# Kernel optimization log

Measured on AMD Instinct MI355X. Metric: run time of the kernel, lower is better.

## Reference

```python
import jax, jax.numpy as jnp
import numpy as np

B, S, H, W = 64, 32, 40, 64
SENS, UNITS, MOTOR, NA = 1283, 48, 4, 2
UNFOLDS = 6  # ncps LTC default ode_unfolds
EPS = 1e-8


def setup_inputs() -> dict:
    key = jax.random.key(0)
    ks = iter(jax.random.split(key, 40))
    u = lambda sh, lo, hi: jax.random.uniform(next(ks), sh, jnp.float32, lo, hi)
    inp = {}
    inp["depth_image"] = jax.random.uniform(next(ks), (B, S, H, W), jnp.float32)
    inp["relative_position"] = jax.random.normal(next(ks), (B, S, 3), jnp.float32)
    # CNN params (conv k3 s2 p1 + ReLU) x3: 1->32->64->32
    def cw(o, i):
        return jax.random.normal(next(ks), (o, i, 3, 3), jnp.float32) / np.sqrt(i * 9.0)
    inp["w1"], inp["b1"] = cw(32, 1), jnp.zeros((32,), jnp.float32)
    inp["w2"], inp["b2"] = cw(64, 32), jnp.zeros((64,), jnp.float32)
    inp["w3"], inp["b3"] = cw(32, 64), jnp.zeros((32,), jnp.float32)
    # LTC cell params (ncps init ranges)
    inp["input_w"] = jnp.ones((SENS,), jnp.float32)
    inp["input_b"] = jnp.zeros((SENS,), jnp.float32)
    inp["sens_w"] = u((SENS, UNITS), 0.001, 1.0)
    inp["sens_mu"] = u((SENS, UNITS), 0.3, 0.8)
    inp["sens_sigma"] = u((SENS, UNITS), 3.0, 8.0)
    inp["sens_erev"] = jnp.sign(jax.random.normal(next(ks), (SENS, UNITS)))
    inp["rec_w"] = u((UNITS, UNITS), 0.001, 1.0)
    inp["rec_mu"] = u((UNITS, UNITS), 0.3, 0.8)
    inp["rec_sigma"] = u((UNITS, UNITS), 3.0, 8.0)
    inp["rec_erev"] = jnp.sign(jax.random.normal(next(ks), (UNITS, UNITS)))
    inp["gleak"] = u((UNITS,), 0.001, 1.0)
    inp["vleak"] = u((UNITS,), -0.2, 0.2)
    inp["cm"] = u((UNITS,), 0.4, 0.6)
    inp["out_w"] = jnp.ones((MOTOR,), jnp.float32)
    inp["out_b"] = jnp.zeros((MOTOR,), jnp.float32)
    inp["head_w"] = jax.random.normal(next(ks), (MOTOR, NA), jnp.float32) * 0.5
    inp["head_b"] = jnp.zeros((NA,), jnp.float32)
    inp["sens_mask"] = (jax.random.uniform(next(ks), (SENS, UNITS)) < 0.3).astype(jnp.int32)
    inp["rec_mask"] = (jax.random.uniform(next(ks), (UNITS, UNITS)) < 0.3).astype(jnp.int32)
    return inp


def _conv(x, w, b):
    y = jax.lax.conv_general_dilated(x, w, (2, 2), [(1, 1), (1, 1)],
                                     dimension_numbers=("NCHW", "OIHW", "NCHW"))
    return jax.nn.relu(y + b[None, :, None, None])


def reference(depth_image, relative_position, w1, b1, w2, b2, w3, b3,
              input_w, input_b, sens_w, sens_mu, sens_sigma, sens_erev,
              rec_w, rec_mu, rec_sigma, rec_erev, gleak, vleak, cm,
              out_w, out_b, head_w, head_b, sens_mask, rec_mask):
    b, s = depth_image.shape[:2]
    x = depth_image.reshape(b * s, 1, H, W)
    x = _conv(_conv(_conv(x, w1, b1), w2, b2), w3, b3)  # [b*s,32,5,8]
    feat = x.reshape(b, s, -1)  # [b,s,1280]
    seq = jnp.concatenate([feat, relative_position.reshape(b, s, -1)], axis=2)  # [b,s,1283]

    sp = jax.nn.softplus
    smask = sens_mask.astype(seq.dtype)
    rmask = rec_mask.astype(seq.dtype)
    cm_t = sp(cm) * UNFOLDS          # cm / (elapsed_time / ode_unfolds), dt=1
    gl = sp(gleak)
    sw_pos = sp(sens_w) * smask
    rw_pos = sp(rec_w) * rmask

    def step(v, xt):  # xt: [b, SENS]
        I = xt * input_w + input_b
        # sensory synapse activations: [b, SENS, UNITS]
        sa = sw_pos * jax.nn.sigmoid(sens_sigma * (I[:, :, None] - sens_mu))
        w_num_s = (sa * sens_erev).sum(1)  # [b, UNITS]
        w_den_s = sa.sum(1)
        def unfold(v, _):
            ra = rw_pos * jax.nn.sigmoid(rec_sigma * (v[:, :, None] - rec_mu))
            num = cm_t * v + gl * vleak + (ra * rec_erev).sum(1) + w_num_s
            den = cm_t + gl + ra.sum(1) + w_den_s
            return num / (den + EPS), None
        v, _ = jax.lax.scan(unfold, v, None, length=UNFOLDS)
        y = v[:, :MOTOR] * out_w + out_b  # motor neuron readout
        return v, y

    v0 = jnp.zeros((b, UNITS), seq.dtype)
    _, ys = jax.lax.scan(step, v0, jnp.swapaxes(seq, 0, 1))  # [s, b, MOTOR]
    pooled = ys.mean(0)  # mean over seq dim
    return jnp.tanh(pooled @ head_w + head_b)  # [b, NA] action mean
```

## Files before the change

### kernel.cpp

```cpp
#include <hip/hip_runtime.h>
#include <hip/hip_bf16.h>


typedef __attribute__((ext_vector_type(8))) short bshort8;
typedef __attribute__((ext_vector_type(4))) float f32x4;

constexpr long OFF_SEQ  = 0;
constexpr long OFF_SP4  = 2627584;
constexpr long OFF_RP4  = 2873920;
constexpr long OFF_CM   = 2886208;
constexpr long OFF_W2B  = 2886400;
constexpr long OFF_W3B  = 2898688;
constexpr long OFF_PART = 2907904;

__device__ __forceinline__ float sp_(float x) {
    return fmaxf(x, 0.f) + log1pf(expf(-fabsf(x)));
}

__global__ void prep_kernel(const float* __restrict__ sens_w, const float* __restrict__ sens_mu,
                            const float* __restrict__ sens_sigma, const float* __restrict__ sens_erev,
                            const int* __restrict__ sens_mask,
                            const float* __restrict__ rec_w, const float* __restrict__ rec_mu,
                            const float* __restrict__ rec_sigma, const float* __restrict__ rec_erev,
                            const int* __restrict__ rec_mask,
                            const float* __restrict__ gleak, const float* __restrict__ vleak,
                            const float* __restrict__ cm,
                            const float* __restrict__ w2, const float* __restrict__ w3,
                            float* __restrict__ ws) {
    const float L2E = 1.4426950408889634f;
    int i = blockIdx.x * 256 + threadIdx.x;
    if (i < 61584) {
        float m  = sens_mask[i] ? 1.f : 0.f;
        float sw = sp_(sens_w[i]) * m;
        float sg = sens_sigma[i], mu = sens_mu[i];
        ((float4*)(ws + OFF_SP4))[i] =
            make_float4(-sg * L2E, sg * mu * L2E, sw * sens_erev[i], sw);
    } else if (i < 64656) {
        int q = i - 61584;
        int j = q >> 6, u = q & 63;
        float4 v = make_float4(0.f, 0.f, 0.f, 0.f);
        if (u < 48) {
            int idx = j * 48 + u;
            float m  = rec_mask[idx] ? 1.f : 0.f;
            float sw = sp_(rec_w[idx]) * m;
            float sg = rec_sigma[idx], mu = rec_mu[idx];
            v = make_float4(-sg * L2E, sg * mu * L2E, sw * rec_erev[idx], sw);
        }
        ((float4*)(ws + OFF_RP4))[q] = v;
    } else if (i < 64704) {
        int u = i - 64656;
        float g = sp_(gleak[u]);
        ws[OFF_CM + u]       = sp_(cm[u]) * 6.f;
        ws[OFF_CM + 64 + u]  = g;
        ws[OFF_CM + 128 + u] = g * vleak[u];
    } else if (i < 89280) {
        int n = i - 64704;
        int j = n & 7, l = (n >> 3) & 63, t2 = n >> 9;
        int wv = t2 & 3;
        int r  = t2 >> 2;
        int xp = r & 1, hk = r >> 1;
        int ky = hk % 3, h = hk / 3;
        int oc = wv * 16 + (l & 15);
        int kgB = l >> 4;
        int icl = (kgB & 1) * 8 + j;
        int ic = h * 16 + icl;
        int kx = 2 * xp + (kgB >> 1);
        float val = (kx == 3) ? 0.f : w2[((oc * 32 + ic) * 3 + ky) * 3 + kx];
        ((__hip_bfloat16*)(ws + OFF_W2B))[n] = __float2bfloat16(val);
    } else if (i < 107712) {
        int n = i - 89280;
        int j = n & 7, l = (n >> 3) & 63, t3 = n >> 9;
        int h = t3 & 1, u2 = t3 >> 1;
        int nt = u2 / 9, p = u2 % 9;
        int ky = p / 3, kx = p % 3;
        int oc = nt * 16 + (l & 15);
        int ic = h * 32 + (l >> 4) * 8 + j;
        ((__hip_bfloat16*)(ws + OFF_W3B))[n] =
            __float2bfloat16(w3[((oc * 64 + ic) * 3 + ky) * 3 + kx]);
    }
}

#define IMGB 0
#define C1H  5424
#define A2E  0
#define A2O  12672
#define SMB  28272

__global__ __launch_bounds__(256, 4) void cnn_kernel(
    const float* __restrict__ depth, const float* __restrict__ relpos,
    const float* __restrict__ w1, const float* __restrict__ b1,
    const float* __restrict__ b2, const float* __restrict__ b3,
    const __hip_bfloat16* __restrict__ w2b, const __hip_bfloat16* __restrict__ w3b,
    float* __restrict__ seq) {
    __shared__ __align__(16) char smraw[SMB];
    const int t = threadIdx.x;
    const int img = blockIdx.x;
    const int l = t & 63;
    const int wvu = __builtin_amdgcn_readfirstlane(t >> 6);
    const int m = l & 15, kg = l >> 4;

    for (int i = t; i < 7068; i += 256) ((uint*)smraw)[i] = 0u;
    __syncthreads();
    for (int i = t; i < 1280; i += 256) {
        int pos = 2 * i;
        int h = pos >> 6, w = pos & 63;
        float2 d = *(const float2*)(depth + (long)img * 2560 + pos);
        __hip_bfloat162 pk = __float22bfloat162_rn(d);
        *(__hip_bfloat162*)(smraw + IMGB + ((h + 1) * 66 + (w + 2)) * 2) = pk;
    }
    __syncthreads();

    const __hip_bfloat16* imgp = (const __hip_bfloat16*)(smraw + IMGB);
    f32x4 acc[10];
    {
        float bias = b2[wvu * 16 + m];
#pragma unroll
        for (int mt = 0; mt < 10; ++mt) acc[mt] = (f32x4){bias, bias, bias, bias};
    }

#pragma unroll 1
    for (int h = 0; h < 2; ++h) {
        const int ocb = h * 16 + wvu * 4;
        float wv4[4][9], bv4[4];
#pragma unroll
        for (int j = 0; j < 4; ++j) {
            bv4[j] = b1[ocb + j];
#pragma unroll
            for (int k = 0; k < 9; ++k) wv4[j][k] = w1[(ocb + j) * 9 + k];
        }
#pragma unroll 1
        for (int i = 0; i < 10; ++i) {
            int p = l + (i << 6);
            int y1 = p >> 5, x1 = p & 31;
            float xin[9];
#pragma unroll
            for (int ky = 0; ky < 3; ++ky)
#pragma unroll
                for (int kx = 0; kx < 3; ++kx)
                    xin[ky * 3 + kx] = __bfloat162float(imgp[(2 * y1 + ky) * 66 + 2 * x1 + kx + 1]);
            float o[4];
#pragma unroll
            for (int j = 0; j < 4; ++j) {
                float a = bv4[j];
#pragma unroll
                for (int k = 0; k < 9; ++k) a = fmaf(wv4[j][k], xin[k], a);
                o[j] = fmaxf(a, 0.f);
            }
            char* cb = smraw + C1H + (((y1 + 1) * 34) + (x1 + 1)) * 32 + wvu * 8;
            *(__hip_bfloat162*)cb       = __float22bfloat162_rn(make_float2(o[0], o[1]));
            *(__hip_bfloat162*)(cb + 4) = __float22bfloat162_rn(make_float2(o[2], o[3]));
        }
        bshort8 Bh[6];
#pragma unroll
        for (int f = 0; f < 6; ++f)
            Bh[f] = *(const bshort8*)(w2b + (((h * 6 + f) * 4 + wvu) * 64 + l) * 8);
        __syncthreads();
#pragma unroll
        for (int ky = 0; ky < 3; ++ky) {
#pragma unroll
            for (int xp = 0; xp < 2; ++xp) {
                bshort8 Bp = Bh[ky * 2 + xp];
                const char* base = smraw + C1H + (ky * 34 + 2 * m + 2 * xp + (kg >> 1)) * 32 + (kg & 1) * 16;
#pragma unroll
                for (int mt = 0; mt < 10; ++mt) {
                    bshort8 A = *(const bshort8*)(base + mt * 2176);
                    acc[mt] = __builtin_amdgcn_mfma_f32_16x16x32_bf16(A, Bp, acc[mt], 0, 0, 0);
                }
            }
        }
        __syncthreads();
    }

    for (int i = t; i < 6336; i += 256) ((uint*)smraw)[i] = 0u;
    __syncthreads();
    {
        int oc = wvu * 16 + m;
        int q = oc >> 3, sub = oc & 7;
#pragma unroll
        for (int mt = 0; mt < 10; ++mt) {
            int row = mt + 1;
#pragma unroll
            for (int reg = 0; reg < 4; ++reg) {
                int x2 = kg * 4 + reg;
                int odd = x2 & 1;
                int xi = odd ? ((x2 + 1) >> 1) : (x2 >> 1);
                char* ab = smraw + (odd ? A2O : A2E);
                float v = fmaxf(acc[mt][reg], 0.f);
                *(__hip_bfloat16*)(ab + (((q * 11 + row) * 9 + xi) * 8 + sub) * 2) = __float2bfloat16(v);
            }
        }
    }
    __syncthreads();

    {
        const int nt = wvu & 1;
        const bool two = wvu < 2;
        f32x4 c3a = (f32x4){0.f, 0.f, 0.f, 0.f};
        f32x4 c3b = (f32x4){0.f, 0.f, 0.f, 0.f};
        const int xb = m & 7, yb = m >> 3;
#pragma unroll
        for (int p = 0; p < 9; ++p) {
            int ky = p / 3, kx = p % 3;
            const char* arr = smraw + ((kx == 1) ? A2E : A2O);
            int xi3 = xb + (kx == 2);
#pragma unroll
            for (int h = 0; h < 2; ++h) {
                bshort8 B = *(const bshort8*)(w3b + (((nt * 9 + p) * 2 + h) * 64 + l) * 8);
                int q = h * 4 + kg;
                const char* base = arr + ((q * 11 + 2 * yb + ky) * 9 + xi3) * 16;
                if (two) {
                    bshort8 A0 = *(const bshort8*)(base);
                    c3a = __builtin_amdgcn_mfma_f32_16x16x32_bf16(A0, B, c3a, 0, 0, 0);
                    bshort8 A2 = *(const bshort8*)(base + 1152);
                    c3b = __builtin_amdgcn_mfma_f32_16x16x32_bf16(A2, B, c3b, 0, 0, 0);
                } else {
                    bshort8 A1 = *(const bshort8*)(base + 576);
                    c3a = __builtin_amdgcn_mfma_f32_16x16x32_bf16(A1, B, c3a, 0, 0, 0);
                }
            }
        }
        __syncthreads();
        float* sb = (float*)smraw;
        int oc = nt * 16 + m;
        float bv = b3[oc];
        int ob40 = oc * 40;
        if (two) {
#pragma unroll
            for (int reg = 0; reg < 4; ++reg) {
                sb[ob40 + kg * 4 + reg] = fmaxf(c3a[reg] + bv, 0.f);
                int px2 = 32 + kg * 4 + reg;
                if (px2 < 40) sb[ob40 + px2] = fmaxf(c3b[reg] + bv, 0.f);
            }
        } else {
#pragma unroll
            for (int reg = 0; reg < 4; ++reg)
                sb[ob40 + 16 + kg * 4 + reg] = fmaxf(c3a[reg] + bv, 0.f);
        }
        __syncthreads();
        for (int i = t; i < 1283; i += 256)
            seq[(long)img * 1283 + i] = (i < 1280) ? sb[i] : relpos[img * 3 + (i - 1280)];
    }
}

__global__ __launch_bounds__(768) void sensory_kernel(
    const float* __restrict__ sp, const float* __restrict__ seq,
    const float* __restrict__ iw, const float* __restrict__ ibias,
    float2* __restrict__ part) {
    const float4* P4 = (const float4*)sp;
    __shared__ __align__(16) char sbuf[49152];
    float*  IT  = (float*)sbuf;
    float2* red = (float2*)sbuf;
    const int t = threadIdx.x;
    const int pb = blockIdx.x * 8;

    for (int p = 0; p < 8; ++p)
        for (int k = t; k < 1283; k += 768)
            IT[k * 8 + p] = fmaf(seq[(long)(pb + p) * 1283 + k], iw[k], ibias[k]);
    __syncthreads();

    const int u = t % 48, kg = t / 48;
    float2 acc[8];
#pragma unroll
    for (int p = 0; p < 8; ++p) acc[p] = make_float2(0.f, 0.f);

#pragma unroll 2
    for (int i = 0; i < 81; ++i) {
        int k = kg + 16 * i;
        if (k < 1283) {
            float4 pv = P4[k * 48 + u];
            float4 Ia = *(const float4*)&IT[k * 8];
            float4 Ib = *(const float4*)&IT[k * 8 + 4];
            float r0 = __builtin_amdgcn_rcpf(1.f + __builtin_amdgcn_exp2f(fmaf(pv.x, Ia.x, pv.y)));
            float r1 = __builtin_amdgcn_rcpf(1.f + __builtin_amdgcn_exp2f(fmaf(pv.x, Ia.y, pv.y)));
            float r2 = __builtin_amdgcn_rcpf(1.f + __builtin_amdgcn_exp2f(fmaf(pv.x, Ia.z, pv.y)));
            float r3 = __builtin_amdgcn_rcpf(1.f + __builtin_amdgcn_exp2f(fmaf(pv.x, Ia.w, pv.y)));
            float r4 = __builtin_amdgcn_rcpf(1.f + __builtin_amdgcn_exp2f(fmaf(pv.x, Ib.x, pv.y)));
            float r5 = __builtin_amdgcn_rcpf(1.f + __builtin_amdgcn_exp2f(fmaf(pv.x, Ib.y, pv.y)));
            float r6 = __builtin_amdgcn_rcpf(1.f + __builtin_amdgcn_exp2f(fmaf(pv.x, Ib.z, pv.y)));
            float r7 = __builtin_amdgcn_rcpf(1.f + __builtin_amdgcn_exp2f(fmaf(pv.x, Ib.w, pv.y)));
            acc[0].x = fmaf(pv.z, r0, acc[0].x); acc[0].y = fmaf(pv.w, r0, acc[0].y);
            acc[1].x = fmaf(pv.z, r1, acc[1].x); acc[1].y = fmaf(pv.w, r1, acc[1].y);
            acc[2].x = fmaf(pv.z, r2, acc[2].x); acc[2].y = fmaf(pv.w, r2, acc[2].y);
            acc[3].x = fmaf(pv.z, r3, acc[3].x); acc[3].y = fmaf(pv.w, r3, acc[3].y);
            acc[4].x = fmaf(pv.z, r4, acc[4].x); acc[4].y = fmaf(pv.w, r4, acc[4].y);
            acc[5].x = fmaf(pv.z, r5, acc[5].x); acc[5].y = fmaf(pv.w, r5, acc[5].y);
            acc[6].x = fmaf(pv.z, r6, acc[6].x); acc[6].y = fmaf(pv.w, r6, acc[6].y);
            acc[7].x = fmaf(pv.z, r7, acc[7].x); acc[7].y = fmaf(pv.w, r7, acc[7].y);
        }
    }
    __syncthreads();
#pragma unroll
    for (int p = 0; p < 8; ++p) red[(kg * 8 + p) * 48 + u] = acc[p];
    __syncthreads();
    if (t < 384) {
        int p = t / 48, uu = t - p * 48;
        float sn = 0.f, sd = 0.f;
#pragma unroll
        for (int g = 0; g < 16; ++g) {
            float2 rr = red[(g * 8 + p) * 48 + uu];
            sn += rr.x; sd += rr.y;
        }
        part[(long)(pb + p) * 48 + uu] = make_float2(sn, sd);
    }
}

__global__ __launch_bounds__(512) void recurrent_kernel(
    const float* __restrict__ rp, const float* __restrict__ cmglv,
    const float2* __restrict__ part,
    const float* __restrict__ out_w, const float* __restrict__ out_b,
    const float* __restrict__ head_w, const float* __restrict__ head_b,
    float* __restrict__ outp) {
    const float4* RP4 = (const float4*)rp;
    __shared__ float2 WL[32 * 48];
    __shared__ float2 red[2][8][64];
    __shared__ float ym[4];
    const int t = threadIdx.x, b = blockIdx.x;
    const int u = t & 63;
    const int jg = __builtin_amdgcn_readfirstlane(t >> 6);
    const int j0 = jg * 6;
    const bool uval = u < 48;
    float4 rpj[6];
#pragma unroll
    for (int jj = 0; jj < 6; ++jj) rpj[jj] = RP4[(j0 + jj) * 64 + u];
    for (int i = t; i < 1536; i += 512) WL[i] = part[(long)b * 1536 + i];
    float cmt = 0.f, gl = 0.f, glv = 0.f;
    if (uval) { cmt = cmglv[u]; gl = cmglv[64 + u]; glv = cmglv[128 + u]; }
    float ow = 0.f, ob = 0.f;
    if (jg == 0 && u < 4) { ow = out_w[u]; ob = out_b[u]; }
    __syncthreads();

    float vn = 0.f;
    float yacc = 0.f;
    int buf = 0;
    for (int s = 0; s < 32; ++s) {
        float2 wnd = uval ? WL[s * 48 + u] : make_float2(0.f, 0.f);
#pragma unroll 1
        for (int unf = 0; unf < 6; ++unf) {
            float pn = 0.f, pd = 0.f;
#pragma unroll
            for (int jj = 0; jj < 6; ++jj) {
                float vj = __shfl(vn, j0 + jj, 64);
                float r = __builtin_amdgcn_rcpf(1.f + __builtin_amdgcn_exp2f(fmaf(rpj[jj].x, vj, rpj[jj].y)));
                pn = fmaf(rpj[jj].z, r, pn);
                pd = fmaf(rpj[jj].w, r, pd);
            }
            red[buf][jg][u] = make_float2(pn, pd);
            __syncthreads();
            float sn = 0.f, sd = 0.f;
#pragma unroll
            for (int g = 0; g < 8; ++g) {
                float2 rr = red[buf][g][u];
                sn += rr.x; sd += rr.y;
            }
            float num = fmaf(cmt, vn, glv) + sn + wnd.x;
            float den = cmt + gl + sd + wnd.y;
            vn = uval ? num / (den + 1e-8f) : 0.f;
            buf ^= 1;
        }
        if (jg == 0 && u < 4) yacc = fmaf(vn, ow, yacc) + ob;
    }
    if (jg == 0 && u < 4) ym[u] = yacc;
    __syncthreads();
    if (t < 2) {
        const float inv = 1.f / 32.f;
        float o = ym[0] * inv * head_w[t] + ym[1] * inv * head_w[2 + t] +
                  ym[2] * inv * head_w[4 + t] + ym[3] * inv * head_w[6 + t] + head_b[t];
        outp[b * 2 + t] = tanhf(o);
    }
}

extern "C" void kernel_launch(void* const* d_in, const int* in_sizes, int n_in,
                              void* d_out, int out_size, void* d_ws, size_t ws_size,
                              hipStream_t stream) {
    const float* depth      = (const float*)d_in[0];
    const float* relpos     = (const float*)d_in[1];
    const float* w1         = (const float*)d_in[2];
    const float* b1         = (const float*)d_in[3];
    const float* w2         = (const float*)d_in[4];
    const float* b2         = (const float*)d_in[5];
    const float* w3         = (const float*)d_in[6];
    const float* b3         = (const float*)d_in[7];
    const float* iw         = (const float*)d_in[8];
    const float* ibias      = (const float*)d_in[9];
    const float* sens_w     = (const float*)d_in[10];
    const float* sens_mu    = (const float*)d_in[11];
    const float* sens_sigma = (const float*)d_in[12];
    const float* sens_erev  = (const float*)d_in[13];
    const float* rec_w      = (const float*)d_in[14];
    const float* rec_mu     = (const float*)d_in[15];
    const float* rec_sigma  = (const float*)d_in[16];
    const float* rec_erev   = (const float*)d_in[17];
    const float* gleak      = (const float*)d_in[18];
    const float* vleak      = (const float*)d_in[19];
    const float* cm         = (const float*)d_in[20];
    const float* out_w      = (const float*)d_in[21];
    const float* out_b      = (const float*)d_in[22];
    const float* head_w     = (const float*)d_in[23];
    const float* head_b     = (const float*)d_in[24];
    const int*   sens_mask  = (const int*)d_in[25];
    const int*   rec_mask   = (const int*)d_in[26];

    float* ws  = (float*)d_ws;
    float* out = (float*)d_out;

    prep_kernel<<<477, 256, 0, stream>>>(sens_w, sens_mu, sens_sigma, sens_erev, sens_mask,
                                         rec_w, rec_mu, rec_sigma, rec_erev, rec_mask,
                                         gleak, vleak, cm, w2, w3, ws);
    cnn_kernel<<<2048, 256, 0, stream>>>(depth, relpos, w1, b1, b2, b3,
                                         (const __hip_bfloat16*)(ws + OFF_W2B),
                                         (const __hip_bfloat16*)(ws + OFF_W3B),
                                         ws + OFF_SEQ);
    sensory_kernel<<<256, 768, 0, stream>>>(ws + OFF_SP4, ws + OFF_SEQ, iw, ibias,
                                            (float2*)(ws + OFF_PART));
    recurrent_kernel<<<64, 512, 0, stream>>>(ws + OFF_RP4, ws + OFF_CM,
                                             (const float2*)(ws + OFF_PART),
                                             out_w, out_b, head_w, head_b, out);
}
```

Measured before the change: 294.7 us.

## Fuse sensory synapse reduction into recurrent kernel and drop partial buffer

Removes the separate sensory kernel and computes the per-timestep sensory numerator and denominator sums inside the recurrent kernel, with each wave handling four timesteps over all 1283 inputs. This eliminates a kernel launch and the global partial-sum write and read. The sensory work now runs on only 64 blocks instead of 256, with a long serial per-thread loop, which reduces parallelism. It also replaces the division in the ODE update with a hardware reciprocal approximation.

```diff
diff --git a/kernel.cpp b/kernel.cpp
--- a/kernel.cpp
+++ b/kernel.cpp
@@ -11,7 +11,6 @@
 constexpr long OFF_CM   = 2886208;
 constexpr long OFF_W2B  = 2886400;
 constexpr long OFF_W3B  = 2898688;
-constexpr long OFF_PART = 2907904;
 
 __device__ __forceinline__ float sp_(float x) {
     return fmaxf(x, 0.f) + log1pf(expf(-fabsf(x)));
@@ -242,75 +241,15 @@
     }
 }
 
-__global__ __launch_bounds__(768) void sensory_kernel(
-    const float* __restrict__ sp, const float* __restrict__ seq,
+__global__ __launch_bounds__(512) void recurrent_kernel(
+    const float* __restrict__ sp4, const float* __restrict__ seq,
     const float* __restrict__ iw, const float* __restrict__ ibias,
-    float2* __restrict__ part) {
-    const float4* P4 = (const float4*)sp;
-    __shared__ __align__(16) char sbuf[49152];
-    float*  IT  = (float*)sbuf;
-    float2* red = (float2*)sbuf;
-    const int t = threadIdx.x;
-    const int pb = blockIdx.x * 8;
-
-    for (int p = 0; p < 8; ++p)
-        for (int k = t; k < 1283; k += 768)
-            IT[k * 8 + p] = fmaf(seq[(long)(pb + p) * 1283 + k], iw[k], ibias[k]);
-    __syncthreads();
-
-    const int u = t % 48, kg = t / 48;
-    float2 acc[8];
-#pragma unroll
-    for (int p = 0; p < 8; ++p) acc[p] = make_float2(0.f, 0.f);
-
-#pragma unroll 2
-    for (int i = 0; i < 81; ++i) {
-        int k = kg + 16 * i;
-        if (k < 1283) {
-            float4 pv = P4[k * 48 + u];
-            float4 Ia = *(const float4*)&IT[k * 8];
-            float4 Ib = *(const float4*)&IT[k * 8 + 4];
-            float r0 = __builtin_amdgcn_rcpf(1.f + __builtin_amdgcn_exp2f(fmaf(pv.x, Ia.x, pv.y)));
-            float r1 = __builtin_amdgcn_rcpf(1.f + __builtin_amdgcn_exp2f(fmaf(pv.x, Ia.y, pv.y)));
-            float r2 = __builtin_amdgcn_rcpf(1.f + __builtin_amdgcn_exp2f(fmaf(pv.x, Ia.z, pv.y)));
-            float r3 = __builtin_amdgcn_rcpf(1.f + __builtin_amdgcn_exp2f(fmaf(pv.x, Ia.w, pv.y)));
-            float r4 = __builtin_amdgcn_rcpf(1.f + __builtin_amdgcn_exp2f(fmaf(pv.x, Ib.x, pv.y)));
-            float r5 = __builtin_amdgcn_rcpf(1.f + __builtin_amdgcn_exp2f(fmaf(pv.x, Ib.y, pv.y)));
-            float r6 = __builtin_amdgcn_rcpf(1.f + __builtin_amdgcn_exp2f(fmaf(pv.x, Ib.z, pv.y)));
-            float r7 = __builtin_amdgcn_rcpf(1.f + __builtin_amdgcn_exp2f(fmaf(pv.x, Ib.w, pv.y)));
-            acc[0].x = fmaf(pv.z, r0, acc[0].x); acc[0].y = fmaf(pv.w, r0, acc[0].y);
-            acc[1].x = fmaf(pv.z, r1, acc[1].x); acc[1].y = fmaf(pv.w, r1, acc[1].y);
-            acc[2].x = fmaf(pv.z, r2, acc[2].x); acc[2].y = fmaf(pv.w, r2, acc[2].y);
-            acc[3].x = fmaf(pv.z, r3, acc[3].x); acc[3].y = fmaf(pv.w, r3, acc[3].y);
-            acc[4].x = fmaf(pv.z, r4, acc[4].x); acc[4].y = fmaf(pv.w, r4, acc[4].y);
-            acc[5].x = fmaf(pv.z, r5, acc[5].x); acc[5].y = fmaf(pv.w, r5, acc[5].y);
-            acc[6].x = fmaf(pv.z, r6, acc[6].x); acc[6].y = fmaf(pv.w, r6, acc[6].y);
-            acc[7].x = fmaf(pv.z, r7, acc[7].x); acc[7].y = fmaf(pv.w, r7, acc[7].y);
-        }
-    }
-    __syncthreads();
-#pragma unroll
-    for (int p = 0; p < 8; ++p) red[(kg * 8 + p) * 48 + u] = acc[p];
-    __syncthreads();
-    if (t < 384) {
-        int p = t / 48, uu = t - p * 48;
-        float sn = 0.f, sd = 0.f;
-#pragma unroll
-        for (int g = 0; g < 16; ++g) {
-            float2 rr = red[(g * 8 + p) * 48 + uu];
-            sn += rr.x; sd += rr.y;
-        }
-        part[(long)(pb + p) * 48 + uu] = make_float2(sn, sd);
-    }
-}
-
-__global__ __launch_bounds__(512) void recurrent_kernel(
     const float* __restrict__ rp, const float* __restrict__ cmglv,
-    const float2* __restrict__ part,
     const float* __restrict__ out_w, const float* __restrict__ out_b,
     const float* __restrict__ head_w, const float* __restrict__ head_b,
     float* __restrict__ outp) {
     const float4* RP4 = (const float4*)rp;
+    const float4* SP4 = (const float4*)sp4;
     __shared__ float2 WL[32 * 48];
     __shared__ float2 red[2][8][64];
     __shared__ float ym[4];
@@ -322,11 +261,40 @@
     float4 rpj[6];
 #pragma unroll
     for (int jj = 0; jj < 6; ++jj) rpj[jj] = RP4[(j0 + jj) * 64 + u];
-    for (int i = t; i < 1536; i += 512) WL[i] = part[(long)b * 1536 + i];
     float cmt = 0.f, gl = 0.f, glv = 0.f;
     if (uval) { cmt = cmglv[u]; gl = cmglv[64 + u]; glv = cmglv[128 + u]; }
     float ow = 0.f, ob = 0.f;
     if (jg == 0 && u < 4) { ow = out_w[u]; ob = out_b[u]; }
+
+    {
+        const float* sq = seq + ((long)b * 32 + jg * 4) * 1283;
+        const int uu = uval ? u : 0;
+        float2 a0 = make_float2(0.f, 0.f), a1 = make_float2(0.f, 0.f);
+        float2 a2 = make_float2(0.f, 0.f), a3 = make_float2(0.f, 0.f);
+#pragma unroll 2
+        for (int k = 0; k < 1283; ++k) {
+            float4 pv = SP4[(long)k * 48 + uu];
+            float wk = iw[k], bk = ibias[k];
+            float I0 = fmaf(sq[k],            wk, bk);
+            float I1 = fmaf(sq[1283 + k],     wk, bk);
+            float I2 = fmaf(sq[2 * 1283 + k], wk, bk);
+            float I3 = fmaf(sq[3 * 1283 + k], wk, bk);
+            float r0 = __builtin_amdgcn_rcpf(1.f + __builtin_amdgcn_exp2f(fmaf(pv.x, I0, pv.y)));
+            float r1 = __builtin_amdgcn_rcpf(1.f + __builtin_amdgcn_exp2f(fmaf(pv.x, I1, pv.y)));
+            float r2 = __builtin_amdgcn_rcpf(1.f + __builtin_amdgcn_exp2f(fmaf(pv.x, I2, pv.y)));
+            float r3 = __builtin_amdgcn_rcpf(1.f + __builtin_amdgcn_exp2f(fmaf(pv.x, I3, pv.y)));
+            a0.x = fmaf(pv.z, r0, a0.x); a0.y = fmaf(pv.w, r0, a0.y);
+            a1.x = fmaf(pv.z, r1, a1.x); a1.y = fmaf(pv.w, r1, a1.y);
+            a2.x = fmaf(pv.z, r2, a2.x); a2.y = fmaf(pv.w, r2, a2.y);
+            a3.x = fmaf(pv.z, r3, a3.x); a3.y = fmaf(pv.w, r3, a3.y);
+        }
+        if (uval) {
+            WL[(jg * 4 + 0) * 48 + u] = a0;
+            WL[(jg * 4 + 1) * 48 + u] = a1;
+            WL[(jg * 4 + 2) * 48 + u] = a2;
+            WL[(jg * 4 + 3) * 48 + u] = a3;
+        }
+    }
     __syncthreads();
 
     float vn = 0.f;
@@ -354,7 +322,7 @@
             }
             float num = fmaf(cmt, vn, glv) + sn + wnd.x;
             float den = cmt + gl + sd + wnd.y;
-            vn = uval ? num / (den + 1e-8f) : 0.f;
+            vn = uval ? num * __builtin_amdgcn_rcpf(den + 1e-8f) : 0.f;
             buf ^= 1;
         }
         if (jg == 0 && u < 4) yacc = fmaf(vn, ow, yacc) + ob;
@@ -410,9 +378,7 @@
                                          (const __hip_bfloat16*)(ws + OFF_W2B),
                                          (const __hip_bfloat16*)(ws + OFF_W3B),
                                          ws + OFF_SEQ);
-    sensory_kernel<<<256, 768, 0, stream>>>(ws + OFF_SP4, ws + OFF_SEQ, iw, ibias,
-                                            (float2*)(ws + OFF_PART));
-    recurrent_kernel<<<64, 512, 0, stream>>>(ws + OFF_RP4, ws + OFF_CM,
-                                             (const float2*)(ws + OFF_PART),
+    recurrent_kernel<<<64, 512, 0, stream>>>(ws + OFF_SP4, ws + OFF_SEQ, iw, ibias,
+                                             ws + OFF_RP4, ws + OFF_CM,
                                              out_w, out_b, head_w, head_b, out);
 }
```

Result: slower. 638.3 us (+116.6%).
